# Performance work log

Measured on AMD Instinct MI355X. Metric: run time of the kernel, lower is better.

Reference implementation:

```python
import jax, jax.numpy as jnp
import numpy as np

NSITES = 262144
ZP1 = 13  # coordination number Z=12, plus the self row


def setup_inputs() -> dict:
    key = jax.random.key(0)
    k1, k2, k3, k4 = jax.random.split(key, 4)
    In = jax.random.normal(k1, (4, 8, NSITES), dtype=jnp.float32)
    NNsites = jax.random.randint(k2, (ZP1, NSITES), 0, NSITES, dtype=jnp.int32)
    Weights = jax.random.normal(k3, (8, 8, 16), dtype=jnp.float32)  # (K, C_out, 2*C_in)
    bias = jax.random.normal(k4, (8, 8), dtype=jnp.float32)         # (K, C_out)
    return {"In": In, "NNsites": NNsites, "Weights": Weights, "bias": bias}


def reference(In, NNsites, Weights, bias):
    # Original math per neighbor z:
    #   total = concat([In, In[:,:,NN[1+z]]], axis=1)            # (B, 2C_in, N)
    #   o[b,n,k,co] = sum_i W[k,co,i]*total[b,i,n] + bias[k,co]
    #   o summed over channels k, then softplus, accumulated over z.
    # Sum over k commutes with the linear map, so use effective weights.
    C_in = In.shape[1]
    Weff = Weights.sum(axis=0)          # (C_out, 2*C_in)
    beff = bias.sum(axis=0)             # (C_out,)
    Ws, Wn = Weff[:, :C_in], Weff[:, C_in:]
    # self contribution, identical for every z
    self_part = jnp.einsum('oi,bin->bon', Ws, In)          # (B, C_out, N)
    # gather all Z neighbor shells at once: (B, C_in, Z, N)
    neigh = In[:, :, NNsites[1:]]
    neigh_out = jnp.einsum('oi,bizn->bozn', Wn, neigh)     # (B, C_out, Z, N)
    pre = self_part[:, :, None, :] + neigh_out + beff[None, :, None, None]
    return jax.nn.softplus(pre).sum(axis=2)                # (B, C_out, N)
```

## Files before the change

### kernel.cpp

```cpp
#include <hip/hip_runtime.h>
#include <hip/hip_fp16.h>

#define NSITES 262144

struct alignas(16) H8 { __half2 h[4]; };
typedef __attribute__((ext_vector_type(2))) float floatx2;
typedef __attribute__((ext_vector_type(4))) unsigned int uintx4;


__global__ __launch_bounds__(256) void prep_kernel(
    const float* __restrict__ In,
    const float* __restrict__ Weights,
    const float* __restrict__ bias,
    uint2* __restrict__ G8,
    H8*    __restrict__ Sp)
{
    __shared__ float ws[8][8], wn[8][8], be[8];
    int t = threadIdx.x;
    if (t < 64) {
        int o = t >> 3, k = t & 7;
        float s0 = 0.f, s1 = 0.f;
        #pragma unroll
        for (int s = 0; s < 8; ++s) {
            s0 += Weights[s*128 + o*16 + k];
            s1 += Weights[s*128 + o*16 + 8 + k];
        }
        ws[o][k] = s0; wn[o][k] = s1;
    } else if (t < 72) {
        int o = t - 64;
        float s = 0.f;
        #pragma unroll
        for (int q = 0; q < 8; ++q) s += bias[q*8 + o];
        be[o] = s;
    }
    __syncthreads();

    int b    = t & 3;
    int sl   = t >> 2;
    int site = blockIdx.x * 64 + sl;

    float x[8];
    #pragma unroll
    for (int i = 0; i < 8; ++i)
        x[i] = In[(b*8 + i) * NSITES + site];

    float g[8], s[8];
    #pragma unroll
    for (int o = 0; o < 8; ++o) {
        float a0 = 0.f, a1 = be[o];
        #pragma unroll
        for (int i = 0; i < 8; ++i) {
            a0 = fmaf(wn[o][i], x[i], a0);
            a1 = fmaf(ws[o][i], x[i], a1);
        }
        g[o] = a0; s[o] = a1;
    }

    unsigned int w0 = 0, w1 = 0;
    w0 = __builtin_amdgcn_cvt_pk_fp8_f32(g[0], g[1], w0, false);
    w0 = __builtin_amdgcn_cvt_pk_fp8_f32(g[2], g[3], w0, true);
    w1 = __builtin_amdgcn_cvt_pk_fp8_f32(g[4], g[5], w1, false);
    w1 = __builtin_amdgcn_cvt_pk_fp8_f32(g[6], g[7], w1, true);
    G8[site*4 + b] = make_uint2(w0, w1);

    H8 sv;
    #pragma unroll
    for (int p = 0; p < 4; ++p) sv.h[p] = __floats2half2_rn(s[2*p], s[2*p+1]);
    Sp[site*4 + b] = sv;
}

__global__ __launch_bounds__(256) void gather_kernel(
    const uintx4* __restrict__ Sp4,
    const uintx4* __restrict__ G16,
    const int*    __restrict__ NN,
    float*        __restrict__ out)
{
    __shared__ float lds[32][129];
    int t    = threadIdx.x;
    int q    = t & 1;
    int sl   = t >> 1;
    int base = blockIdx.x * 128;
    int n    = base + sl;

    uintx4 sw0 = __builtin_nontemporal_load(Sp4 + n*4 + 2*q);
    uintx4 sw1 = __builtin_nontemporal_load(Sp4 + n*4 + 2*q + 1);
    float sp[16];
    #pragma unroll
    for (int p = 0; p < 4; ++p) {
        unsigned int wa = sw0[p], wb = sw1[p];
        __half2 ha, hb;
        __builtin_memcpy(&ha, &wa, 4);
        __builtin_memcpy(&hb, &wb, 4);
        float2 fa = __half22float2(ha), fb = __half22float2(hb);
        sp[2*p]     = fa.x; sp[2*p+1]     = fa.y;
        sp[8 + 2*p] = fb.x; sp[8 + 2*p+1] = fb.y;
    }

    int m[12];
    #pragma unroll
    for (int z = 0; z < 12; ++z)
        m[z] = __builtin_nontemporal_load(&NN[(z+1) * NSITES + n]);

    const float NLOG2E = -1.44269504f;
    float acc[16], prod[16];
    #pragma unroll
    for (int k = 0; k < 16; ++k) { acc[k] = 0.f; prod[k] = 1.f; }

    #pragma unroll
    for (int zz = 0; zz < 2; ++zz) {
        uintx4 gw[6];
        #pragma unroll
        for (int z = 0; z < 6; ++z)
            gw[z] = G16[(size_t)m[zz*6 + z] * 2 + q];
        #pragma unroll
        for (int z = 0; z < 6; ++z) {
            float g[16];
            #pragma unroll
            for (int p = 0; p < 4; ++p) {
                floatx2 lo = __builtin_amdgcn_cvt_pk_f32_fp8(gw[z][p], false);
                floatx2 hi = __builtin_amdgcn_cvt_pk_f32_fp8(gw[z][p], true);
                g[4*p]   = lo[0]; g[4*p+1] = lo[1];
                g[4*p+2] = hi[0]; g[4*p+3] = hi[1];
            }
            #pragma unroll
            for (int k = 0; k < 16; ++k) {
                float x  = sp[k] + g[k];
                float ax = fabsf(x);
                acc[k] += fmaxf(x, 0.f);
                float e = __builtin_amdgcn_exp2f(ax * NLOG2E);
                prod[k] = fmaf(prod[k], e, prod[k]);
            }
        }
    }

    #pragma unroll
    for (int k = 0; k < 16; ++k)
        lds[q*16 + k][sl] = acc[k] + 0.69314718f * __builtin_amdgcn_logf(prod[k]);
    __syncthreads();

    int s  = t & 127;
    int j0 = t >> 7;
    #pragma unroll
    for (int r = 0; r < 16; ++r) {
        int j = j0*16 + r;
        __builtin_nontemporal_store(lds[j][s], &out[j * NSITES + base + s]);
    }
}

extern "C" void kernel_launch(void* const* d_in, const int* in_sizes, int n_in,
                              void* d_out, int out_size, void* d_ws, size_t ws_size,
                              hipStream_t stream) {
    const float* In      = (const float*)d_in[0];
    const int*   NN      = (const int*)  d_in[1];
    const float* Weights = (const float*)d_in[2];
    const float* bias    = (const float*)d_in[3];
    float* out = (float*)d_out;

    uint2*  G8  = (uint2*)d_ws;
    H8*     Sp  = (H8*)((char*)d_ws + (size_t)NSITES * 32);
    uintx4* G16 = (uintx4*)G8;
    uintx4* Sp4 = (uintx4*)Sp;

    prep_kernel<<<NSITES / 64, 256, 0, stream>>>(In, Weights, bias, G8, Sp);
    gather_kernel<<<NSITES / 128, 256, 0, stream>>>(Sp4, G16, NN, out);
}
```

Baseline: 138.3 us.

## Split gather work across four lanes per site with two sites per thread

The gather kernel now assigns four lanes per site, one per batch element, and each thread handles two sites 64 apart. Before, two lanes per site each covered two batches. Each neighbor gather becomes an 8-byte load instead of a 16-byte one, and each thread issues twice as many independent loads, which is meant to raise memory-level parallelism for the random gathers. The trade-off is more NN index loads per thread and more, smaller gather transactions. The LDS padding is changed to 133 to avoid bank conflicts with the new write pattern.

```diff
diff --git a/kernel.cpp b/kernel.cpp
--- a/kernel.cpp
+++ b/kernel.cpp
@@ -71,20 +71,21 @@
 
 __global__ __launch_bounds__(256) void gather_kernel(
     const uintx4* __restrict__ Sp4,
-    const uintx4* __restrict__ G16,
+    const uint2*  __restrict__ G8,
     const int*    __restrict__ NN,
     float*        __restrict__ out)
 {
-    __shared__ float lds[32][129];
+    __shared__ float lds[32][133];
     int t    = threadIdx.x;
-    int q    = t & 1;
-    int sl   = t >> 1;
+    int q    = t & 3;
+    int sl   = t >> 2;
     int base = blockIdx.x * 128;
-    int n    = base + sl;
+    int n0   = base + sl;
+    int n1   = base + 64 + sl;
 
-    uintx4 sw0 = __builtin_nontemporal_load(Sp4 + n*4 + 2*q);
-    uintx4 sw1 = __builtin_nontemporal_load(Sp4 + n*4 + 2*q + 1);
-    float sp[16];
+    uintx4 sw0 = __builtin_nontemporal_load(Sp4 + n0*4 + q);
+    uintx4 sw1 = __builtin_nontemporal_load(Sp4 + n1*4 + q);
+    float sp0[8], sp1[8];
     #pragma unroll
     for (int p = 0; p < 4; ++p) {
         unsigned int wa = sw0[p], wb = sw1[p];
@@ -92,50 +93,64 @@
         __builtin_memcpy(&ha, &wa, 4);
         __builtin_memcpy(&hb, &wb, 4);
         float2 fa = __half22float2(ha), fb = __half22float2(hb);
-        sp[2*p]     = fa.x; sp[2*p+1]     = fa.y;
-        sp[8 + 2*p] = fb.x; sp[8 + 2*p+1] = fb.y;
+        sp0[2*p] = fa.x; sp0[2*p+1] = fa.y;
+        sp1[2*p] = fb.x; sp1[2*p+1] = fb.y;
     }
 
-    int m[12];
+    int m0[12], m1[12];
     #pragma unroll
-    for (int z = 0; z < 12; ++z)
-        m[z] = __builtin_nontemporal_load(&NN[(z+1) * NSITES + n]);
+    for (int z = 0; z < 12; ++z) {
+        m0[z] = __builtin_nontemporal_load(&NN[(z+1) * NSITES + n0]);
+        m1[z] = __builtin_nontemporal_load(&NN[(z+1) * NSITES + n1]);
+    }
 
     const float NLOG2E = -1.44269504f;
-    float acc[16], prod[16];
+    float acc0[8], prod0[8], acc1[8], prod1[8];
     #pragma unroll
-    for (int k = 0; k < 16; ++k) { acc[k] = 0.f; prod[k] = 1.f; }
+    for (int k = 0; k < 8; ++k) {
+        acc0[k] = 0.f; prod0[k] = 1.f;
+        acc1[k] = 0.f; prod1[k] = 1.f;
+    }
 
     #pragma unroll
-    for (int zz = 0; zz < 2; ++zz) {
-        uintx4 gw[6];
+    for (int zz = 0; zz < 4; ++zz) {
+        uint2 g0[3], g1[3];
         #pragma unroll
-        for (int z = 0; z < 6; ++z)
-            gw[z] = G16[(size_t)m[zz*6 + z] * 2 + q];
+        for (int j = 0; j < 3; ++j) {
+            g0[j] = G8[(size_t)m0[zz*3 + j] * 4 + q];
+            g1[j] = G8[(size_t)m1[zz*3 + j] * 4 + q];
+        }
         #pragma unroll
-        for (int z = 0; z < 6; ++z) {
-            float g[16];
+        for (int j = 0; j < 3; ++j) {
+            float ga[8], gb[8];
+            floatx2 p;
+            p = __builtin_amdgcn_cvt_pk_f32_fp8(g0[j].x, false); ga[0]=p[0]; ga[1]=p[1];
+            p = __builtin_amdgcn_cvt_pk_f32_fp8(g0[j].x, true ); ga[2]=p[0]; ga[3]=p[1];
+            p = __builtin_amdgcn_cvt_pk_f32_fp8(g0[j].y, false); ga[4]=p[0]; ga[5]=p[1];
+            p = __builtin_amdgcn_cvt_pk_f32_fp8(g0[j].y, true ); ga[6]=p[0]; ga[7]=p[1];
+            p = __builtin_amdgcn_cvt_pk_f32_fp8(g1[j].x, false); gb[0]=p[0]; gb[1]=p[1];
+            p = __builtin_amdgcn_cvt_pk_f32_fp8(g1[j].x, true ); gb[2]=p[0]; gb[3]=p[1];
+            p = __builtin_amdgcn_cvt_pk_f32_fp8(g1[j].y, false); gb[4]=p[0]; gb[5]=p[1];
+            p = __builtin_amdgcn_cvt_pk_f32_fp8(g1[j].y, true ); gb[6]=p[0]; gb[7]=p[1];
             #pragma unroll
-            for (int p = 0; p < 4; ++p) {
-                floatx2 lo = __builtin_amdgcn_cvt_pk_f32_fp8(gw[z][p], false);
-                floatx2 hi = __builtin_amdgcn_cvt_pk_f32_fp8(gw[z][p], true);
-                g[4*p]   = lo[0]; g[4*p+1] = lo[1];
-                g[4*p+2] = hi[0]; g[4*p+3] = hi[1];
-            }
-            #pragma unroll
-            for (int k = 0; k < 16; ++k) {
-                float x  = sp[k] + g[k];
-                float ax = fabsf(x);
-                acc[k] += fmaxf(x, 0.f);
-                float e = __builtin_amdgcn_exp2f(ax * NLOG2E);
-                prod[k] = fmaf(prod[k], e, prod[k]);
+            for (int k = 0; k < 8; ++k) {
+                float xa  = sp0[k] + ga[k];
+                float axa = fabsf(xa);
+                acc0[k] += fmaxf(xa, 0.f);
+                prod0[k] = fmaf(prod0[k], __builtin_amdgcn_exp2f(axa * NLOG2E), prod0[k]);
+                float xb  = sp1[k] + gb[k];
+                float axb = fabsf(xb);
+                acc1[k] += fmaxf(xb, 0.f);
+                prod1[k] = fmaf(prod1[k], __builtin_amdgcn_exp2f(axb * NLOG2E), prod1[k]);
             }
         }
     }
 
     #pragma unroll
-    for (int k = 0; k < 16; ++k)
-        lds[q*16 + k][sl] = acc[k] + 0.69314718f * __builtin_amdgcn_logf(prod[k]);
+    for (int k = 0; k < 8; ++k) {
+        lds[q*8 + k][sl]      = acc0[k] + 0.69314718f * __builtin_amdgcn_logf(prod0[k]);
+        lds[q*8 + k][sl + 64] = acc1[k] + 0.69314718f * __builtin_amdgcn_logf(prod1[k]);
+    }
     __syncthreads();
 
     int s  = t & 127;
@@ -158,9 +173,8 @@
 
     uint2*  G8  = (uint2*)d_ws;
     H8*     Sp  = (H8*)((char*)d_ws + (size_t)NSITES * 32);
-    uintx4* G16 = (uintx4*)G8;
     uintx4* Sp4 = (uintx4*)Sp;
 
     prep_kernel<<<NSITES / 64, 256, 0, stream>>>(In, Weights, bias, G8, Sp);
-    gather_kernel<<<NSITES / 128, 256, 0, stream>>>(Sp4, G16, NN, out);
+    gather_kernel<<<NSITES / 128, 256, 0, stream>>>(Sp4, G8, NN, out);
 }
```

Result: slower. 141.6 us (+2.4%).
